# Kernel tuning notes

Hardware: AMD Instinct MI355X
Metric: run time of the kernel (lower is better)

Reference implementation:

```python
import jax, jax.numpy as jnp
import numpy as np

L, P, D, AL = 48, 2048, 50, 5
ONEHOT = 5 * D + 5  # 255, leaf one-hot size per encode()


def setup_inputs() -> dict:
    rng = np.random.default_rng(0)
    # node types: 0=leaf 1=unary 2=exist 3=univ 4=binary 5=functor 6=predicate
    node_type = np.zeros((L, P), np.int64)
    node_type[1:] = rng.integers(0, 7, size=(L - 1, P))
    children = -np.ones((L, P, AL), np.int64)
    for l in range(1, L):
        hi = l * P  # children must come from earlier levels (topological order)
        nt = node_type[l]
        n_child = np.where(nt == 0, 0,
                  np.where(nt <= 3, 1,
                  np.where(nt == 4, 2, rng.integers(1, AL + 1, size=P))))
        samp = rng.integers(0, hi, size=(P, AL))
        m = np.arange(AL)[None, :] < n_child[:, None]
        children[l] = np.where(m, samp, -1)
    # two-hot leaf encoding per encode(): v[category]=1 (0..4) and v[i+5]=1
    cat = rng.integers(0, 5, size=(L, P))
    ident = rng.integers(0, 5 * D, size=(L, P))
    onehot = np.zeros((L, P, ONEHOT), np.float32)
    li, pi = np.meshgrid(np.arange(L), np.arange(P), indexing='ij')
    onehot[li, pi, ident + 5] = 1.0
    onehot[li, pi, cat] = 1.0

    def lin(i, out_d, in_d):
        k = jax.random.fold_in(jax.random.key(0), i)
        kw, kb = jax.random.split(k)
        W = jax.random.normal(kw, (out_d, in_d), jnp.float32) * (in_d ** -0.5)
        b = jax.random.normal(kb, (out_d,), jnp.float32) * 0.01
        return W, b

    W_leaf, b_leaf = lin(0, D, ONEHOT)
    W_unary, b_unary = lin(1, D, D)
    W_exist, b_exist = lin(2, D, D)
    W_univ, b_univ = lin(3, D, D)
    W_bin, b_bin = lin(4, D, 3 * D)
    W_fun, b_fun = lin(5, D, (1 + AL) * D)
    W_pred, b_pred = lin(6, D, (1 + AL) * D)
    W_final, b_final = lin(7, ONEHOT, D)
    return dict(node_type=jnp.asarray(node_type, jnp.int32),
                children=jnp.asarray(children, jnp.int32),
                onehot=jnp.asarray(onehot),
                W_leaf=W_leaf, b_leaf=b_leaf, W_unary=W_unary, b_unary=b_unary,
                W_exist=W_exist, b_exist=b_exist, W_univ=W_univ, b_univ=b_univ,
                W_bin=W_bin, b_bin=b_bin, W_fun=W_fun, b_fun=b_fun,
                W_pred=W_pred, b_pred=b_pred, W_final=W_final, b_final=b_final)


def reference(node_type, children, onehot,
              W_leaf, b_leaf, W_unary, b_unary, W_exist, b_exist,
              W_univ, b_univ, W_bin, b_bin, W_fun, b_fun,
              W_pred, b_pred, W_final, b_final):
    relu = jax.nn.relu

    def step(buf, xs):
        l, nt, ch, oh = xs  # nt:[P], ch:[P,AL], oh:[P,ONEHOT]
        leaf = relu(oh @ W_leaf.T + b_leaf)                      # relu(leaf_net(onehot))
        mask = (ch >= 0).astype(buf.dtype)[..., None]
        ce = buf[jnp.clip(ch, 0)] * mask                          # [P,AL,D] child embeddings
        c0, c1 = ce[:, 0], ce[:, 1]
        unary = relu(c0 @ W_unary.T + b_unary)
        exist = relu(c0 @ W_exist.T + b_exist)
        univ = relu(c0 @ W_univ.T + b_univ)
        binv = relu(jnp.concatenate([c0, leaf, c1], -1) @ W_bin.T + b_bin)  # cat[left, op, right]
        fin = jnp.concatenate([leaf, ce.reshape(P, AL * D)], -1)  # [P,(1+AL)*D]
        fun = relu(fin @ W_fun.T + b_fun)
        pred = relu(fin @ W_pred.T + b_pred)
        outs = jnp.stack([leaf, unary, exist, univ, binv, fun, pred])  # [7,P,D]
        out = jnp.take_along_axis(outs, nt[None, :, None], axis=0)[0]
        buf = jax.lax.dynamic_update_slice(buf, out, (l * P, 0))
        return buf, None

    buf0 = jnp.zeros((L * P, D), onehot.dtype)
    xs = (jnp.arange(L), node_type, children, onehot)
    buf, _ = jax.lax.scan(step, buf0, xs)
    root = buf[-1]
    return root @ W_final.T + b_final  # self.final(self.visit(input)), shape [255]
```

## Files before the change

kernel.cpp:

```cpp
#include <hip/hip_runtime.h>

#define L_ 48
#define P_ 2048
#define D_ 50
#define AL_ 5
#define OH_ 255
#define NNODES (L_*P_)
#define MAXN_ 256
#define HSZ 1024
#define NTHREADS 512
#define NWAVES 8
#define SPIN_BOUND (1 << 24)

__device__ __forceinline__ void pfl(const void* g, void* lds_scratch) {
    __builtin_amdgcn_global_load_lds(
        (const __attribute__((address_space(1))) unsigned int*)g,
        (__attribute__((address_space(3))) unsigned int*)lds_scratch,
        4, 0, 0);
}

__device__ __forceinline__ float dot50L(const float* __restrict__ Wg, const float* inL) {
    const float4* x4 = (const float4*)inL;
    float a0 = 0.f, a1 = 0.f, a2 = 0.f, a3 = 0.f;
    #pragma unroll
    for (int q = 0; q < 12; ++q) {
        float4 x = x4[q];
        float2 w0 = *(const float2*)(Wg + q * 4);
        float2 w1 = *(const float2*)(Wg + q * 4 + 2);
        a0 += w0.x * x.x; a1 += w0.y * x.y;
        a2 += w1.x * x.z; a3 += w1.y * x.w;
    }
    float4 xt = x4[12];
    float2 wt = *(const float2*)(Wg + 48);
    a0 += wt.x * xt.x; a1 += wt.y * xt.y;
    return (a0 + a1) + (a2 + a3);
}

__device__ __forceinline__ float dotrow(const float* __restrict__ W, const float* in, int len) {
    float a0 = 0.f, a1 = 0.f, a2 = 0.f, a3 = 0.f;
    int j = 0;
    for (; j + 4 <= len; j += 4) {
        a0 += W[j] * in[j]; a1 += W[j+1] * in[j+1];
        a2 += W[j+2] * in[j+2]; a3 += W[j+3] * in[j+3];
    }
    for (; j < len; ++j) a0 += W[j] * in[j];
    return (a0 + a1) + (a2 + a3);
}

__device__ __forceinline__ float pf4(const float* __restrict__ p, int n, int t, int nth) {
    float s = 0.f;
    for (int i = t * 4; i + 3 < n; i += nth * 4) {
        float4 v = *reinterpret_cast<const float4*>(p + i);
        s += v.x + v.y + v.z + v.w;
    }
    return s;
}

__global__ __launch_bounds__(NTHREADS)
void formula_kernel(const int* __restrict__ node_type,
                    const int* __restrict__ children,
                    const float* __restrict__ onehot,
                    const float* __restrict__ W_leaf,  const float* __restrict__ b_leaf,
                    const float* __restrict__ W_unary, const float* __restrict__ b_unary,
                    const float* __restrict__ W_exist, const float* __restrict__ b_exist,
                    const float* __restrict__ W_univ,  const float* __restrict__ b_univ,
                    const float* __restrict__ W_bin,   const float* __restrict__ b_bin,
                    const float* __restrict__ W_fun,   const float* __restrict__ b_fun,
                    const float* __restrict__ W_pred,  const float* __restrict__ b_pred,
                    const float* __restrict__ W_final, const float* __restrict__ b_final,
                    float* __restrict__ out)
{
    __shared__ int h_key[HSZ];
    __shared__ int h_val[HSZ];
    __shared__ int list[MAXN_];
    __shared__ int nt_l[MAXN_];
    __shared__ int order[MAXN_];
    __shared__ int rdy[MAXN_];
    __shared__ int ch_l[MAXN_][AL_];
    __shared__ int cnt_sh;
    __shared__ __align__(16) float emb_s[MAXN_][52];
    __shared__ __align__(16) float lrow[NWAVES][52];
    __shared__ int   nzj[NWAVES][16];
    __shared__ float nzv[NWAVES][16];
    __shared__ unsigned pfscr[64];

    const int tid  = threadIdx.x;
    const int lane = tid & 63;
    const int wave = tid >> 6;

    if (wave == 0) {
        for (int i = lane; i < HSZ; i += 64) h_key[i] = -1;
        __builtin_amdgcn_wave_barrier();
        if (lane == 0) {
            cnt_sh = 1;
            const int root = NNODES - 1;
            list[0] = root;
            unsigned h = ((unsigned)root * 2654435761u) >> 16;
            for (;;) { int i = (int)(h & (HSZ - 1));
                       if (h_key[i] == -1) { h_key[i] = root; h_val[i] = 0; break; } ++h; }
            pfl(&node_type[root], pfscr);
            const char* ohb = (const char*)(onehot + (size_t)root * OH_);
            #pragma unroll
            for (int q = 0; q < 16; ++q) pfl(ohb + q * 64, pfscr);
            pfl(ohb + 1016, pfscr);
        }
        __builtin_amdgcn_wave_barrier();

        int total_reg = 1;
        int fs = 0, fe = 1;
        for (int round = 0; round < 48 && fs < fe; ++round) {
            const int npairs = (fe - fs) * AL_;
            int ic = 0;
            for (int base = 0; base < npairs; base += 256) {
                const int m = (npairs - base < 256) ? (npairs - base) : 256;
                int cv[4];
                #pragma unroll
                for (int u = 0; u < 4; ++u) {
                    int t = base + lane + u * 64;
                    cv[u] = (t < base + m)
                        ? children[(size_t)list[fs + t / AL_] * AL_ + (t % AL_)] : -1;
                }
                #pragma unroll
                for (int u = 0; u < 4; ++u) {
                    int c = cv[u];
                    if (c >= 0) {
                        unsigned h = ((unsigned)c * 2654435761u) >> 16;
                        for (;;) {
                            int i = (int)(h & (HSZ - 1));
                            int prev = atomicCAS(&h_key[i], -1, c);
                            if (prev == -1) {
                                int pos = atomicAdd(&cnt_sh, 1);
                                h_val[i] = pos;
                                if (pos < MAXN_) list[pos] = c;
                                ic++;
                                const char* chb = (const char*)&children[(size_t)c * AL_];
                                pfl(chb, pfscr); pfl(chb + 16, pfscr);
                                pfl(&node_type[c], pfscr);
                                const char* ohb = (const char*)(onehot + (size_t)c * OH_);
                                #pragma unroll
                                for (int q = 0; q < 16; ++q) pfl(ohb + q * 64, pfscr);
                                pfl(ohb + 1016, pfscr);
                                break;
                            }
                            if (prev == c) break;
                            ++h;
                        }
                    }
                }
            }
            __builtin_amdgcn_wave_barrier();
            int tot = ic;
            #pragma unroll
            for (int d = 1; d < 64; d <<= 1) tot += __shfl_xor(tot, d);
            total_reg += tot;
            fs = fe;
            fe = (total_reg < MAXN_) ? total_reg : MAXN_;
            __builtin_amdgcn_wave_barrier();
        }
    } else {
        const int t = tid - 64, nth = NTHREADS - 64;
        float s = 0.f;
        s += pf4(W_leaf,  D_ * OH_,    t, nth);
        s += pf4(W_unary, D_ * D_,     t, nth);
        s += pf4(W_exist, D_ * D_,     t, nth);
        s += pf4(W_univ,  D_ * D_,     t, nth);
        s += pf4(W_bin,   D_ * 3 * D_, t, nth);
        s += pf4(W_fun,   D_ * 6 * D_, t, nth);
        s += pf4(W_pred,  D_ * 6 * D_, t, nth);
        s += pf4(W_final, OH_ * D_,    t, nth);
        if (t < 64) {
            s += b_leaf[t % D_] + b_unary[t % D_] + b_exist[t % D_] + b_univ[t % D_]
               + b_bin[t % D_] + b_fun[t % D_] + b_pred[t % D_] + b_final[t];
        }
        asm volatile("" :: "v"(s));
    }
    __syncthreads();

    const int count = (cnt_sh < MAXN_) ? cnt_sh : MAXN_;

    for (int t = tid; t < count * 6; t += NTHREADS) {
        int i = t / 6, j = t % 6;
        int n = list[i];
        if (j == 0) {
            nt_l[i] = node_type[n];
        } else {
            int c = children[(size_t)n * AL_ + (j - 1)];
            int sl = -1;
            if (c >= 0) {
                unsigned h = ((unsigned)c * 2654435761u) >> 16;
                for (;;) {
                    int ii = (int)(h & (HSZ - 1));
                    if (h_key[ii] == c) { sl = h_val[ii]; break; }
                    ++h;
                }
                if (sl >= MAXN_) sl = -1;
            }
            ch_l[i][j - 1] = sl;
        }
    }
    for (int i = tid; i < count; i += NTHREADS) {
        int me = list[i];
        int r = 0;
        for (int j = 0; j < count; ++j) r += (list[j] < me);
        order[r] = i;
        rdy[i] = 0;
    }
    __syncthreads();

    volatile int* vrdy = rdy;
    for (int pos = wave; pos < count; pos += NWAVES) {
        const int slot = order[pos];
        const int nt = nt_l[slot];
        const int n = list[slot];

        float leafv = 0.0f;
        if (nt == 0 || nt >= 4) {
            const float* oh = onehot + (size_t)n * OH_;
            float v[4]; int c2 = 0;
            #pragma unroll
            for (int t = 0; t < 4; ++t) {
                int j = lane * 4 + t;
                v[t] = (j < OH_) ? oh[j] : 0.0f;
                if (v[t] != 0.0f) c2++;
            }
            int incl = c2;
            #pragma unroll
            for (int dlt = 1; dlt < 64; dlt <<= 1) {
                int o = __shfl_up(incl, dlt);
                if (lane >= dlt) incl += o;
            }
            const int excl = incl - c2;
            const int total = __shfl(incl, 63);
            if (total <= 16) {
                int p2 = excl;
                #pragma unroll
                for (int t = 0; t < 4; ++t)
                    if (v[t] != 0.0f) { nzj[wave][p2] = lane * 4 + t; nzv[wave][p2] = v[t]; p2++; }
            }
            __builtin_amdgcn_wave_barrier();
            if (lane < D_) {
                float sacc = b_leaf[lane];
                if (total <= 16) {
                    for (int i2 = 0; i2 < total; ++i2)
                        sacc += nzv[wave][i2] * W_leaf[lane * OH_ + nzj[wave][i2]];
                } else {
                    sacc += dotrow(W_leaf + lane * OH_, oh, OH_);
                }
                leafv = fmaxf(sacc, 0.0f);
                if (nt >= 4) lrow[wave][lane] = leafv;
            }
            __builtin_amdgcn_wave_barrier();
        }

        float outv = 0.0f;
        if (nt == 0) {
            outv = leafv;
        } else {
            #pragma unroll
            for (int k = 0; k < AL_; ++k) {
                int cs = ch_l[slot][k];
                if (cs >= 0) {
                    int guard = 0;
                    while (vrdy[cs] == 0 && guard < SPIN_BOUND) {
                        __builtin_amdgcn_s_sleep(1);
                        ++guard;
                    }
                }
            }
            __threadfence_block();
            if (lane < D_) {
                float s;
                if (nt <= 3) {
                    const float* W = (nt == 1) ? W_unary : (nt == 2) ? W_exist : W_univ;
                    const float* b = (nt == 1) ? b_unary : (nt == 2) ? b_exist : b_univ;
                    s = b[lane];
                    const int cs0 = ch_l[slot][0];
                    if (cs0 >= 0) s += dot50L(W + lane * D_, emb_s[cs0]);
                } else if (nt == 4) {
                    const float* W = W_bin + lane * 3 * D_;
                    s = b_bin[lane];
                    const int cs0 = ch_l[slot][0], cs1 = ch_l[slot][1];
                    if (cs0 >= 0) s += dot50L(W, emb_s[cs0]);
                    s += dot50L(W + D_, lrow[wave]);
                    if (cs1 >= 0) s += dot50L(W + 2 * D_, emb_s[cs1]);
                } else {
                    const float* W = ((nt == 5) ? W_fun : W_pred) + lane * 6 * D_;
                    s = ((nt == 5) ? b_fun : b_pred)[lane] + dot50L(W, lrow[wave]);
                    #pragma unroll
                    for (int k = 0; k < AL_; ++k) {
                        int cs = ch_l[slot][k];
                        if (cs >= 0) s += dot50L(W + (1 + k) * D_, emb_s[cs]);
                    }
                }
                outv = fmaxf(s, 0.0f);
            }
        }
        if (lane < D_) emb_s[slot][lane] = outv;
        __threadfence_block();
        if (lane == 0) vrdy[slot] = 1;
    }
    __syncthreads();

    const int rootslot = order[count - 1];
    for (int o = tid; o < OH_; o += NTHREADS)
        out[o] = b_final[o] + dot50L(W_final + o * D_, emb_s[rootslot]);
}

extern "C" void kernel_launch(void* const* d_in, const int* in_sizes, int n_in,
                              void* d_out, int out_size, void* d_ws, size_t ws_size,
                              hipStream_t stream) {
    const int*   node_type = (const int*)d_in[0];
    const int*   children  = (const int*)d_in[1];
    const float* onehot    = (const float*)d_in[2];
    const float* W_leaf  = (const float*)d_in[3];  const float* b_leaf  = (const float*)d_in[4];
    const float* W_unary = (const float*)d_in[5];  const float* b_unary = (const float*)d_in[6];
    const float* W_exist = (const float*)d_in[7];  const float* b_exist = (const float*)d_in[8];
    const float* W_univ  = (const float*)d_in[9];  const float* b_univ  = (const float*)d_in[10];
    const float* W_bin   = (const float*)d_in[11]; const float* b_bin   = (const float*)d_in[12];
    const float* W_fun   = (const float*)d_in[13]; const float* b_fun   = (const float*)d_in[14];
    const float* W_pred  = (const float*)d_in[15]; const float* b_pred  = (const float*)d_in[16];
    const float* W_final = (const float*)d_in[17]; const float* b_final = (const float*)d_in[18];

    float* out = (float*)d_out;

    formula_kernel<<<1, NTHREADS, 0, stream>>>(
        node_type, children, onehot,
        W_leaf, b_leaf, W_unary, b_unary, W_exist, b_exist, W_univ, b_univ,
        W_bin, b_bin, W_fun, b_fun, W_pred, b_pred, W_final, b_final,
        out);
}
```

Before: 26.48 us.

## Hoist leaf nets out of dependency chain, stage unary weights in LDS, overlap prefetch

```diff
diff --git a/kernel.cpp b/kernel.cpp
--- a/kernel.cpp
+++ b/kernel.cpp
@@ -7,17 +7,10 @@
 #define OH_ 255
 #define NNODES (L_*P_)
 #define MAXN_ 256
-#define HSZ 1024
+#define HSZ 512
 #define NTHREADS 512
 #define NWAVES 8
-#define SPIN_BOUND (1 << 24)
-
-__device__ __forceinline__ void pfl(const void* g, void* lds_scratch) {
-    __builtin_amdgcn_global_load_lds(
-        (const __attribute__((address_space(1))) unsigned int*)g,
-        (__attribute__((address_space(3))) unsigned int*)lds_scratch,
-        4, 0, 0);
-}
+#define SPIN_BOUND (1 << 22)
 
 __device__ __forceinline__ float dot50L(const float* __restrict__ Wg, const float* inL) {
     const float4* x4 = (const float4*)inL;
@@ -32,6 +25,22 @@
     }
     float4 xt = x4[12];
     float2 wt = *(const float2*)(Wg + 48);
+    a0 += wt.x * xt.x; a1 += wt.y * xt.y;
+    return (a0 + a1) + (a2 + a3);
+}
+
+__device__ __forceinline__ float dot50LL(const float* WL, const float* xL) {
+    const float4* w4 = (const float4*)WL;
+    const float4* x4 = (const float4*)xL;
+    float a0 = 0.f, a1 = 0.f, a2 = 0.f, a3 = 0.f;
+    #pragma unroll
+    for (int q = 0; q < 12; ++q) {
+        float4 w = w4[q], x = x4[q];
+        a0 += w.x * x.x; a1 += w.y * x.y;
+        a2 += w.z * x.z; a3 += w.w * x.w;
+    }
+    float2 wt = *(const float2*)(WL + 48);
+    float2 xt = *(const float2*)(xL + 48);
     a0 += wt.x * xt.x; a1 += wt.y * xt.y;
     return (a0 + a1) + (a2 + a3);
 }
@@ -77,69 +86,54 @@
     __shared__ int order[MAXN_];
     __shared__ int rdy[MAXN_];
     __shared__ int ch_l[MAXN_][AL_];
-    __shared__ int cnt_sh;
+    __shared__ int cnt_sh, done_sh;
     __shared__ __align__(16) float emb_s[MAXN_][52];
-    __shared__ __align__(16) float lrow[NWAVES][52];
+    __shared__ __align__(16) float leaf_s[MAXN_][52];
+    __shared__ __align__(16) float W_lds[3][D_][52];
     __shared__ int   nzj[NWAVES][16];
     __shared__ float nzv[NWAVES][16];
-    __shared__ unsigned pfscr[64];
 
     const int tid  = threadIdx.x;
     const int lane = tid & 63;
     const int wave = tid >> 6;
 
+    h_key[tid & (HSZ - 1)] = -1;
+    if (tid == 0) { cnt_sh = 1; done_sh = 0; list[0] = NNODES - 1; }
+    __syncthreads();
+
     if (wave == 0) {
-        for (int i = lane; i < HSZ; i += 64) h_key[i] = -1;
-        __builtin_amdgcn_wave_barrier();
         if (lane == 0) {
-            cnt_sh = 1;
             const int root = NNODES - 1;
-            list[0] = root;
             unsigned h = ((unsigned)root * 2654435761u) >> 16;
             for (;;) { int i = (int)(h & (HSZ - 1));
                        if (h_key[i] == -1) { h_key[i] = root; h_val[i] = 0; break; } ++h; }
-            pfl(&node_type[root], pfscr);
-            const char* ohb = (const char*)(onehot + (size_t)root * OH_);
-            #pragma unroll
-            for (int q = 0; q < 16; ++q) pfl(ohb + q * 64, pfscr);
-            pfl(ohb + 1016, pfscr);
         }
         __builtin_amdgcn_wave_barrier();
 
         int total_reg = 1;
         int fs = 0, fe = 1;
-        for (int round = 0; round < 48 && fs < fe; ++round) {
-            const int npairs = (fe - fs) * AL_;
+        while (fs < fe) {
             int ic = 0;
-            for (int base = 0; base < npairs; base += 256) {
-                const int m = (npairs - base < 256) ? (npairs - base) : 256;
-                int cv[4];
+            for (int i = fs + lane; i < fe; i += 64) {
+                int n = list[i];
+                int cv[AL_];
                 #pragma unroll
-                for (int u = 0; u < 4; ++u) {
-                    int t = base + lane + u * 64;
-                    cv[u] = (t < base + m)
-                        ? children[(size_t)list[fs + t / AL_] * AL_ + (t % AL_)] : -1;
-                }
+                for (int k = 0; k < AL_; ++k) cv[k] = children[(size_t)n * AL_ + k];
                 #pragma unroll
-                for (int u = 0; u < 4; ++u) {
-                    int c = cv[u];
+                for (int k = 0; k < AL_; ++k) ch_l[i][k] = cv[k];
+                #pragma unroll
+                for (int k = 0; k < AL_; ++k) {
+                    int c = cv[k];
                     if (c >= 0) {
                         unsigned h = ((unsigned)c * 2654435761u) >> 16;
                         for (;;) {
-                            int i = (int)(h & (HSZ - 1));
-                            int prev = atomicCAS(&h_key[i], -1, c);
+                            int s2 = (int)(h & (HSZ - 1));
+                            int prev = atomicCAS(&h_key[s2], -1, c);
                             if (prev == -1) {
                                 int pos = atomicAdd(&cnt_sh, 1);
-                                h_val[i] = pos;
+                                h_val[s2] = pos;
                                 if (pos < MAXN_) list[pos] = c;
                                 ic++;
-                                const char* chb = (const char*)&children[(size_t)c * AL_];
-                                pfl(chb, pfscr); pfl(chb + 16, pfscr);
-                                pfl(&node_type[c], pfscr);
-                                const char* ohb = (const char*)(onehot + (size_t)c * OH_);
-                                #pragma unroll
-                                for (int q = 0; q < 16; ++q) pfl(ohb + q * 64, pfscr);
-                                pfl(ohb + 1016, pfscr);
                                 break;
                             }
                             if (prev == c) break;
@@ -157,49 +151,71 @@
             fe = (total_reg < MAXN_) ? total_reg : MAXN_;
             __builtin_amdgcn_wave_barrier();
         }
+        if (lane == 0) *((volatile int*)&done_sh) = 1;
+    } else if (wave == 1) {
+        float s = 0.f;
+        if (lane < D_) s += b_leaf[lane] + b_unary[lane] + b_exist[lane] + b_univ[lane]
+                          + b_bin[lane] + b_fun[lane] + b_pred[lane];
+        for (int j = lane; j < OH_; j += 64) s += b_final[j];
+        volatile int* vc = &cnt_sh;
+        volatile int* vd = &done_sh;
+        int seen = 0;
+        for (;;) {
+            int done = *vd;
+            int c = *vc;
+            if (c > MAXN_) c = MAXN_;
+            for (int i = seen; i < c; ++i) {
+                int n = list[i];
+                if ((unsigned)n >= (unsigned)NNODES) n = 0;
+                const float* oh = onehot + (size_t)n * OH_;
+                if (lane < 63) {
+                    int j = lane * 4;
+                    s += oh[j] + oh[j+1] + oh[j+2] + oh[j+3];
+                } else {
+                    s += (float)node_type[n];
+                }
+            }
+            seen = c;
+            if (done) break;
+        }
+        asm volatile("" :: "v"(s));
     } else {
-        const int t = tid - 64, nth = NTHREADS - 64;
+        const int t = tid - 128, nth = NTHREADS - 128;
+        for (int e = t; e < 3 * D_ * D_; e += nth) {
+            int m = e / (D_ * D_), r = e % (D_ * D_);
+            const float* Wm = (m == 0) ? W_unary : (m == 1) ? W_exist : W_univ;
+            W_lds[m][r / D_][r % D_] = Wm[r];
+        }
         float s = 0.f;
         s += pf4(W_leaf,  D_ * OH_,    t, nth);
-        s += pf4(W_unary, D_ * D_,     t, nth);
-        s += pf4(W_exist, D_ * D_,     t, nth);
-        s += pf4(W_univ,  D_ * D_,     t, nth);
         s += pf4(W_bin,   D_ * 3 * D_, t, nth);
         s += pf4(W_fun,   D_ * 6 * D_, t, nth);
         s += pf4(W_pred,  D_ * 6 * D_, t, nth);
         s += pf4(W_final, OH_ * D_,    t, nth);
-        if (t < 64) {
-            s += b_leaf[t % D_] + b_unary[t % D_] + b_exist[t % D_] + b_univ[t % D_]
-               + b_bin[t % D_] + b_fun[t % D_] + b_pred[t % D_] + b_final[t];
-        }
         asm volatile("" :: "v"(s));
     }
     __syncthreads();
 
     const int count = (cnt_sh < MAXN_) ? cnt_sh : MAXN_;
 
-    for (int t = tid; t < count * 6; t += NTHREADS) {
-        int i = t / 6, j = t % 6;
-        int n = list[i];
-        if (j == 0) {
-            nt_l[i] = node_type[n];
-        } else {
-            int c = children[(size_t)n * AL_ + (j - 1)];
+    for (int t = tid; t < count * AL_; t += NTHREADS) {
+        int i = t / AL_, k = t % AL_;
+        int c = ch_l[i][k];
+        if (c >= 0) {
             int sl = -1;
-            if (c >= 0) {
-                unsigned h = ((unsigned)c * 2654435761u) >> 16;
-                for (;;) {
-                    int ii = (int)(h & (HSZ - 1));
-                    if (h_key[ii] == c) { sl = h_val[ii]; break; }
-                    ++h;
-                }
-                if (sl >= MAXN_) sl = -1;
-            }
-            ch_l[i][j - 1] = sl;
+            unsigned h = ((unsigned)c * 2654435761u) >> 16;
+            for (;;) {
+                int ii = (int)(h & (HSZ - 1));
+                if (h_key[ii] == c) { sl = h_val[ii]; break; }
+                ++h;
+            }
+            if (sl >= MAXN_) sl = -1;
+            ch_l[i][k] = sl;
         }
     }
     for (int i = tid; i < count; i += NTHREADS) {
         int me = list[i];
+        nt_l[i] = node_type[me];
         int r = 0;
         for (int j = 0; j < count; ++j) r += (list[j] < me);
         order[r] = i;
@@ -207,93 +223,91 @@
     }
     __syncthreads();
 
+    for (int slot = wave; slot < count; slot += NWAVES) {
+        const int nt = nt_l[slot];
+        if (nt >= 1 && nt <= 3) continue;
+        const int n = list[slot];
+        const float* oh = onehot + (size_t)n * OH_;
+        float v[4]; int c2 = 0;
+        #pragma unroll
+        for (int t = 0; t < 4; ++t) {
+            int j = lane * 4 + t;
+            v[t] = (j < OH_) ? oh[j] : 0.0f;
+            if (v[t] != 0.0f) c2++;
+        }
+        int incl = c2;
+        #pragma unroll
+        for (int dlt = 1; dlt < 64; dlt <<= 1) {
+            int o = __shfl_up(incl, dlt);
+            if (lane >= dlt) incl += o;
+        }
+        const int excl = incl - c2;
+        const int total = __shfl(incl, 63);
+        if (total <= 16) {
+            int p2 = excl;
+            #pragma unroll
+            for (int t = 0; t < 4; ++t)
+                if (v[t] != 0.0f) { nzj[wave][p2] = lane * 4 + t; nzv[wave][p2] = v[t]; p2++; }
+        }
+        __builtin_amdgcn_wave_barrier();
+        if (lane < D_) {
+            float sacc = b_leaf[lane];
+            if (total <= 16) {
+                for (int i2 = 0; i2 < total; ++i2)
+                    sacc += nzv[wave][i2] * W_leaf[lane * OH_ + nzj[wave][i2]];
+            } else {
+                sacc += dotrow(W_leaf + lane * OH_, oh, OH_);
+            }
+            float lv = fmaxf(sacc, 0.0f);
+            if (nt == 0) { emb_s[slot][lane] = lv; }
+            else         { leaf_s[slot][lane] = lv; }
+        }
+        if (nt == 0 && lane == 0) rdy[slot] = 1;
+        __builtin_amdgcn_wave_barrier();
+    }
+    __syncthreads();
+
     volatile int* vrdy = rdy;
     for (int pos = wave; pos < count; pos += NWAVES) {
         const int slot = order[pos];
         const int nt = nt_l[slot];
-        const int n = list[slot];
-
-        float leafv = 0.0f;
-        if (nt == 0 || nt >= 4) {
-            const float* oh = onehot + (size_t)n * OH_;
-            float v[4]; int c2 = 0;
-            #pragma unroll
-            for (int t = 0; t < 4; ++t) {
-                int j = lane * 4 + t;
-                v[t] = (j < OH_) ? oh[j] : 0.0f;
-                if (v[t] != 0.0f) c2++;
-            }
-            int incl = c2;
-            #pragma unroll
-            for (int dlt = 1; dlt < 64; dlt <<= 1) {
-                int o = __shfl_up(incl, dlt);
-                if (lane >= dlt) incl += o;
-            }
-            const int excl = incl - c2;
-            const int total = __shfl(incl, 63);
-            if (total <= 16) {
-                int p2 = excl;
+        if (nt == 0) continue;
+
+        #pragma unroll
+        for (int k = 0; k < AL_; ++k) {
+            int cs = ch_l[slot][k];
+            if (cs >= 0) {
+                int guard = 0;
+                while (vrdy[cs] == 0 && guard < SPIN_BOUND) ++guard;
+            }
+        }
+        __threadfence_block();
+
+        float outv = 0.0f;
+        if (lane < D_) {
+            float s;
+            if (nt <= 3) {
+                const float* b = (nt == 1) ? b_unary : (nt == 2) ? b_exist : b_univ;
+                s = b[lane];
+                const int cs0 = ch_l[slot][0];
+                if (cs0 >= 0) s += dot50LL(W_lds[nt - 1][lane], emb_s[cs0]);
+            } else if (nt == 4) {
+                const float* W = W_bin + lane * 3 * D_;
+                s = b_bin[lane];
+                const int cs0 = ch_l[slot][0], cs1 = ch_l[slot][1];
+                if (cs0 >= 0) s += dot50L(W, emb_s[cs0]);
+                s += dot50L(W + D_, leaf_s[slot]);
+                if (cs1 >= 0) s += dot50L(W + 2 * D_, emb_s[cs1]);
+            } else {
+                const float* W = ((nt == 5) ? W_fun : W_pred) + lane * 6 * D_;
+                s = ((nt == 5) ? b_fun : b_pred)[lane] + dot50L(W, leaf_s[slot]);
                 #pragma unroll
-                for (int t = 0; t < 4; ++t)
-                    if (v[t] != 0.0f) { nzj[wave][p2] = lane * 4 + t; nzv[wave][p2] = v[t]; p2++; }
-            }
-            __builtin_amdgcn_wave_barrier();
-            if (lane < D_) {
-                float sacc = b_leaf[lane];
-                if (total <= 16) {
-                    for (int i2 = 0; i2 < total; ++i2)
-                        sacc += nzv[wave][i2] * W_leaf[lane * OH_ + nzj[wave][i2]];
-                } else {
-                    sacc += dotrow(W_leaf + lane * OH_, oh, OH_);
+                for (int k = 0; k < AL_; ++k) {
+                    int cs = ch_l[slot][k];
+                    if (cs >= 0) s += dot50L(W + (1 + k) * D_, emb_s[cs]);
                 }
-                leafv = fmaxf(sacc, 0.0f);
-                if (nt >= 4) lrow[wave][lane] = leafv;
-            }
-            __builtin_amdgcn_wave_barrier();
-        }
-
-        float outv = 0.0f;
-        if (nt == 0) {
-            outv = leafv;
-        } else {
-            #pragma unroll
-            for (int k = 0; k < AL_; ++k) {
-                int cs = ch_l[slot][k];
-                if (cs >= 0) {
-                    int guard = 0;
-                    while (vrdy[cs] == 0 && guard < SPIN_BOUND) {
-                        __builtin_amdgcn_s_sleep(1);
-                        ++guard;
-                    }
-                }
-            }
-            __threadfence_block();
-            if (lane < D_) {
-                float s;
-                if (nt <= 3) {
-                    const float* W = (nt == 1) ? W_unary : (nt == 2) ? W_exist : W_univ;
-                    const float* b = (nt == 1) ? b_unary : (nt == 2) ? b_exist : b_univ;
-                    s = b[lane];
-                    const int cs0 = ch_l[slot][0];
-                    if (cs0 >= 0) s += dot50L(W + lane * D_, emb_s[cs0]);
-                } else if (nt == 4) {
-                    const float* W = W_bin + lane * 3 * D_;
-                    s = b_bin[lane];
-                    const int cs0 = ch_l[slot][0], cs1 = ch_l[slot][1];
-                    if (cs0 >= 0) s += dot50L(W, emb_s[cs0]);
-                    s += dot50L(W + D_, lrow[wave]);
-                    if (cs1 >= 0) s += dot50L(W + 2 * D_, emb_s[cs1]);
-                } else {
-                    const float* W = ((nt == 5) ? W_fun : W_pred) + lane * 6 * D_;
-                    s = ((nt == 5) ? b_fun : b_pred)[lane] + dot50L(W, lrow[wave]);
-                    #pragma unroll
-                    for (int k = 0; k < AL_; ++k) {
-                        int cs = ch_l[slot][k];
-                        if (cs >= 0) s += dot50L(W + (1 + k) * D_, emb_s[cs]);
-                    }
-                }
-                outv = fmaxf(s, 0.0f);
-            }
+            }
+            outv = fmaxf(s, 0.0f);
         }
         if (lane < D_) emb_s[slot][lane] = outv;
         __threadfence_block();
```

Measured after the change: 24.13 us. 1.1x faster.
